# Performance work log

Hardware: AMD Instinct MI355X
Metric: run time of the kernel (lower is better)

## Reference

```python
import jax, jax.numpy as jnp
import numpy as np

EPS = 1e-5


def conv1d(x, w, b):
    # x: (B, C_in, S), w: (C_out, C_in, K), 'same' padding = K//2
    pad = w.shape[-1] // 2
    y = jax.lax.conv_general_dilated(
        x, w, window_strides=(1,), padding=[(pad, pad)],
        dimension_numbers=("NCH", "OIH", "NCH"))
    return y + b[None, :, None]


def layer_norm(x, g, b):
    m = jnp.mean(x, axis=-1, keepdims=True)
    v = jnp.var(x, axis=-1, keepdims=True)
    return (x - m) * jax.lax.rsqrt(v + EPS) * g + b


def duration_predict(x, conv1_w, conv1_b, conv2_w, conv2_b,
                     ln1_g, ln1_b, ln2_g, ln2_b, lin_w, lin_b):
    # x: (B, S, C)
    out = conv1d(jnp.swapaxes(x, -2, -1), conv1_w, conv1_b)          # (B, F, S)
    out = jax.nn.relu(layer_norm(jnp.swapaxes(out, -2, -1), ln1_g, ln1_b))  # (B, S, F)
    out = conv1d(jnp.swapaxes(out, -2, -1), conv2_w, conv2_b)        # (B, F, S)
    out = jax.nn.relu(layer_norm(jnp.swapaxes(out, -2, -1), ln2_g, ln2_b))  # (B, S, F)
    out = jax.nn.relu(out @ lin_w.T + lin_b)                          # (B, S, 1)
    return jnp.squeeze(out, -1)                                       # (B, S)


def setup_inputs() -> dict:
    key = jax.random.key(0)
    ks = jax.random.split(key, 6)
    B, S, C = 16, 1024, 256
    F_, K = 256, 3
    inp = {
        "x": jax.random.normal(ks[0], (B, S, C), dtype=jnp.float32),
        "target": jax.random.uniform(ks[1], (B, S), dtype=jnp.float32),
        "conv1_w": jax.random.normal(ks[2], (F_, C, K), dtype=jnp.float32) * 0.02,
        "conv1_b": jnp.zeros((F_,), dtype=jnp.float32),
        "conv2_w": jax.random.normal(ks[3], (F_, F_, K), dtype=jnp.float32) * 0.02,
        "conv2_b": jnp.zeros((F_,), dtype=jnp.float32),
        "ln1_g": jnp.ones((F_,), dtype=jnp.float32),
        "ln1_b": jnp.zeros((F_,), dtype=jnp.float32),
        "ln2_g": jnp.ones((F_,), dtype=jnp.float32),
        "ln2_b": jnp.zeros((F_,), dtype=jnp.float32),
        "lin_w": jax.random.normal(ks[4], (1, F_), dtype=jnp.float32) * 0.02,
        "lin_b": jnp.zeros((1,), dtype=jnp.float32),
    }
    return inp


def reference(x, target, conv1_w, conv1_b, conv2_w, conv2_b,
              ln1_g, ln1_b, ln2_g, ln2_b, lin_w, lin_b):
    reg_len = duration_predict(x, conv1_w, conv1_b, conv2_w, conv2_b,
                               ln1_g, ln1_b, ln2_g, ln2_b, lin_w, lin_b)
    # Faithful to the original: max_len uses exp(target), the mask uses round(target).
    # max_len is data-dependent -> computed from concrete target (host-side, like the original).
    max_len = int(np.round(float(jnp.max(jnp.sum(jnp.exp(target), axis=-1)))))
    d = jnp.round(target)                 # (B, S) integer-valued durations (banker's rounding, like Python round)
    fin = jnp.cumsum(d, axis=-1)          # (B, S) end offsets
    start = fin - d                       # (B, S) start offsets
    t = jnp.arange(max_len, dtype=target.dtype)  # (T,)
    mask = ((t[None, None, :] >= start[..., None]) &
            (t[None, None, :] < fin[..., None])).astype(x.dtype)  # (B, S, T)
    # x.transpose @ mask -> (B, C, T) -> transpose -> (B, T, C)
    expanded = jnp.einsum("bsc,bst->btc", x, mask)
    return expanded, reg_len
```

## Files before the change

### kernel.cpp

```cpp
#include <hip/hip_runtime.h>
#include <hip/hip_bf16.h>

using frag_ab = __attribute__((ext_vector_type(8))) short;
using frag_cd = __attribute__((ext_vector_type(4))) float;

#define SLEN 1024
#define CDIM 256
#define KTOT 768
#define PD 8

static __device__ __forceinline__ short f2bf(float f) {
    __hip_bfloat16 h = __float2bfloat16(f);
    return *reinterpret_cast<short*>(&h);
}

__global__ __launch_bounds__(1024) void scan_repack_kernel(
    const float* __restrict__ target, int* __restrict__ src, int T,
    const float* __restrict__ w1, __hip_bfloat16* __restrict__ bt1,
    const float* __restrict__ w2, __hip_bfloat16* __restrict__ bt2)
{
    __shared__ int waveSum[16];
    const int tid = threadIdx.x;

    if (blockIdx.x < 16) {
        const int b = blockIdx.x;
        for (int i = tid; i < T; i += 1024) src[b * T + i] = -1;

        const float tv = target[b * SLEN + tid];
        const int d = (int)rintf(tv);

        const int lane = tid & 63;
        const int wid = tid >> 6;
        int v = d;
#pragma unroll
        for (int off = 1; off < 64; off <<= 1) {
            int n = __shfl_up(v, off);
            if (lane >= off) v += n;
        }
        if (lane == 63) waveSum[wid] = v;
        __syncthreads();
        if (tid < 16) {
            int wv = waveSum[tid];
#pragma unroll
            for (int off = 1; off < 16; off <<= 1) {
                int n = __shfl_up(wv, off);
                if (tid >= off) wv += n;
            }
            waveSum[tid] = wv;
        }
        __syncthreads();
        const int fin = v + (wid > 0 ? waveSum[wid - 1] : 0);
        const int start = fin - d;
        for (int t = start; t < fin; ++t)
            if (t >= 0 && t < T) src[b * T + t] = tid;
    } else {
        const int id = (blockIdx.x - 16) * 1024 + tid;
        const int which = id >= 196608;
        const int e = which ? id - 196608 : id;
        const int f = e / KTOT;
        const int K = e - f * KTOT;
        const int k3 = K >> 8;
        const int c = K & 255;
        const float* w = which ? w2 : w1;
        __hip_bfloat16* bt = which ? bt2 : bt1;
        bt[f * KTOT + K] = __float2bfloat16(w[f * KTOT + c * 3 + k3]);
    }
}

__global__ __launch_bounds__(512, 2) void fused_conv_expand(
    const float* __restrict__ x,
    const __hip_bfloat16* __restrict__ bt1,
    const __hip_bfloat16* __restrict__ bt2,
    const float* __restrict__ cb1, const float* __restrict__ g1, const float* __restrict__ be1,
    const float* __restrict__ cb2, const float* __restrict__ g2, const float* __restrict__ be2,
    const float* __restrict__ lw, const float* __restrict__ lb,
    float* __restrict__ reg_len,
    const int* __restrict__ src, float* __restrict__ expanded, int T)
{
    __shared__ __align__(16) unsigned char xt[68 * 512];
    __shared__ __align__(16) unsigned char yt[66 * 512];
    __shared__ float red[66][17];
    __shared__ float stats[66][2];

    const int tid = threadIdx.x;
    const int lane = tid & 63;
    const int wid = tid >> 6;

    if (blockIdx.x >= 256) {
        const int row = (blockIdx.x - 256) * 8 + wid;
        const int nrows = 16 * T;
        if (row < nrows) {
            const int b = row / T;
            const int s = src[row];
            float4 val = make_float4(0.f, 0.f, 0.f, 0.f);
            if (s >= 0)
                val = *(const float4*)(x + ((size_t)(b * SLEN + s)) * CDIM + lane * 4);
            *(float4*)(expanded + (size_t)row * CDIM + lane * 4) = val;
        }
        return;
    }

    const int b = blockIdx.x >> 4;
    const int sx = blockIdx.x & 15;
    const int s0 = sx * 64;

    const int l15 = lane & 15;
    const int lk = lane >> 4;
    const int fbase = wid * 32;

    const __hip_bfloat16* p10 = bt1 + (size_t)(fbase + l15) * KTOT + lk * 8;
    const __hip_bfloat16* p11 = p10 + 16 * KTOT;
    frag_ab pb0[PD], pb1[PD];
#pragma unroll
    for (int i = 0; i < PD; ++i) {
        pb0[i] = *(const frag_ab*)(p10 + i * 32);
        pb1[i] = *(const frag_ab*)(p11 + i * 32);
    }

    const float* xin = x + (size_t)b * SLEN * CDIM;
    for (int ii = tid; ii < 68 * 32; ii += 512) {
        const int r = ii >> 5, cc = ii & 31;
        const int s = s0 - 2 + r;
        frag_ab v = {0, 0, 0, 0, 0, 0, 0, 0};
        if (s >= 0 && s < SLEN) {
            const float4* p = (const float4*)(xin + (size_t)s * CDIM + cc * 8);
            const float4 q0 = p[0], q1 = p[1];
            v[0] = f2bf(q0.x); v[1] = f2bf(q0.y); v[2] = f2bf(q0.z); v[3] = f2bf(q0.w);
            v[4] = f2bf(q1.x); v[5] = f2bf(q1.y); v[6] = f2bf(q1.z); v[7] = f2bf(q1.w);
        }
        *(frag_ab*)(xt + r * 512 + ((cc * 16) ^ ((r & 7) << 4))) = v;
    }
    __syncthreads();

    frag_cd acc1[5][2];
#pragma unroll
    for (int mf = 0; mf < 5; ++mf) {
        acc1[mf][0] = {0.f, 0.f, 0.f, 0.f};
        acc1[mf][1] = {0.f, 0.f, 0.f, 0.f};
    }
#pragma unroll
    for (int kk = 0; kk < 24; ++kk) {
        const frag_ab bb0 = pb0[kk % PD];
        const frag_ab bb1 = pb1[kk % PD];
        if (kk + PD < 24) {
            pb0[kk % PD] = *(const frag_ab*)(p10 + (kk + PD) * 32);
            pb1[kk % PD] = *(const frag_ab*)(p11 + (kk + PD) * 32);
        }
        const int k3 = kk >> 3;
        const int colbyte = (kk & 7) * 64 + lk * 16;
        frag_ab a[5];
#pragma unroll
        for (int mf = 0; mf < 5; ++mf) {
            int r = mf * 16 + l15 + k3;
            if (mf == 4) r = (r > 67) ? 67 : r;
            a[mf] = *(const frag_ab*)(xt + r * 512 + (colbyte ^ ((r & 7) << 4)));
        }
#pragma unroll
        for (int mf = 0; mf < 5; ++mf) {
            acc1[mf][0] = __builtin_amdgcn_mfma_f32_16x16x32_bf16(a[mf], bb0, acc1[mf][0], 0, 0, 0);
            acc1[mf][1] = __builtin_amdgcn_mfma_f32_16x16x32_bf16(a[mf], bb1, acc1[mf][1], 0, 0, 0);
        }
    }

    const __hip_bfloat16* p20 = bt2 + (size_t)(fbase + l15) * KTOT + lk * 8;
    const __hip_bfloat16* p21 = p20 + 16 * KTOT;
    frag_ab qb0[PD], qb1[PD];
#pragma unroll
    for (int i = 0; i < PD; ++i) {
        qb0[i] = *(const frag_ab*)(p20 + i * 32);
        qb1[i] = *(const frag_ab*)(p21 + i * 32);
    }

    {
        const float bias0 = cb1[fbase + l15];
        const float bias1 = cb1[fbase + 16 + l15];
#pragma unroll
        for (int mf = 0; mf < 5; ++mf) {
#pragma unroll
            for (int j = 0; j < 4; ++j) {
                acc1[mf][0][j] += bias0;
                acc1[mf][1][j] += bias1;
                float p = acc1[mf][0][j] + acc1[mf][1][j];
                float q = acc1[mf][0][j] * acc1[mf][0][j] + acc1[mf][1][j] * acc1[mf][1][j];
#pragma unroll
                for (int m = 1; m < 16; m <<= 1) {
                    p += __shfl_xor(p, m);
                    q += __shfl_xor(q, m);
                }
                const bool valid = (mf < 4) || (lk == 0 && j < 2);
                if (l15 == 0 && valid) {
                    const int yr = mf * 16 + lk * 4 + j;
                    red[yr][wid * 2] = p;
                    red[yr][wid * 2 + 1] = q;
                }
            }
        }
    }
    __syncthreads();
    if (tid < 66) {
        float s = 0.f, q = 0.f;
#pragma unroll
        for (int wv = 0; wv < 8; ++wv) { s += red[tid][wv * 2]; q += red[tid][wv * 2 + 1]; }
        const float mean = s * (1.f / 256.f);
        const float var = q * (1.f / 256.f) - mean * mean;
        stats[tid][0] = mean;
        stats[tid][1] = rsqrtf(var + 1e-5f);
    }
    __syncthreads();

    {
        const float ga0 = g1[fbase + l15], ga1 = g1[fbase + 16 + l15];
        const float bb0 = be1[fbase + l15], bb1 = be1[fbase + 16 + l15];
        const int c0b = (fbase + l15) * 2;
        const int c1b = (fbase + 16 + l15) * 2;
#pragma unroll
        for (int mf = 0; mf < 5; ++mf) {
#pragma unroll
            for (int j = 0; j < 4; ++j) {
                const bool valid = (mf < 4) || (lk == 0 && j < 2);
                if (valid) {
                    const int yr = mf * 16 + lk * 4 + j;
                    const float mean = stats[yr][0], rs = stats[yr][1];
                    float v0 = fmaxf((acc1[mf][0][j] - mean) * rs * ga0 + bb0, 0.f);
                    float v1 = fmaxf((acc1[mf][1][j] - mean) * rs * ga1 + bb1, 0.f);
                    const bool zrow = (sx == 0 && yr == 0) || (sx == 15 && yr == 65);
                    if (zrow) { v0 = 0.f; v1 = 0.f; }
                    const int sw = (yr & 7) << 4;
                    *(short*)(yt + yr * 512 + (c0b ^ sw)) = f2bf(v0);
                    *(short*)(yt + yr * 512 + (c1b ^ sw)) = f2bf(v1);
                }
            }
        }
    }
    __syncthreads();

    frag_cd acc2[4][2];
#pragma unroll
    for (int mf = 0; mf < 4; ++mf) {
        acc2[mf][0] = {0.f, 0.f, 0.f, 0.f};
        acc2[mf][1] = {0.f, 0.f, 0.f, 0.f};
    }
#pragma unroll
    for (int kk = 0; kk < 24; ++kk) {
        const frag_ab bb0 = qb0[kk % PD];
        const frag_ab bb1 = qb1[kk % PD];
        if (kk + PD < 24) {
            qb0[kk % PD] = *(const frag_ab*)(p20 + (kk + PD) * 32);
            qb1[kk % PD] = *(const frag_ab*)(p21 + (kk + PD) * 32);
        }
        const int k3 = kk >> 3;
        const int colbyte = (kk & 7) * 64 + lk * 16;
        frag_ab a[4];
#pragma unroll
        for (int mf = 0; mf < 4; ++mf) {
            const int r = mf * 16 + l15 + k3;
            a[mf] = *(const frag_ab*)(yt + r * 512 + (colbyte ^ ((r & 7) << 4)));
        }
#pragma unroll
        for (int mf = 0; mf < 4; ++mf) {
            acc2[mf][0] = __builtin_amdgcn_mfma_f32_16x16x32_bf16(a[mf], bb0, acc2[mf][0], 0, 0, 0);
            acc2[mf][1] = __builtin_amdgcn_mfma_f32_16x16x32_bf16(a[mf], bb1, acc2[mf][1], 0, 0, 0);
        }
    }

    {
        const float bias0 = cb2[fbase + l15];
        const float bias1 = cb2[fbase + 16 + l15];
#pragma unroll
        for (int mf = 0; mf < 4; ++mf) {
#pragma unroll
            for (int j = 0; j < 4; ++j) {
                acc2[mf][0][j] += bias0;
                acc2[mf][1][j] += bias1;
                float p = acc2[mf][0][j] + acc2[mf][1][j];
                float q = acc2[mf][0][j] * acc2[mf][0][j] + acc2[mf][1][j] * acc2[mf][1][j];
#pragma unroll
                for (int m = 1; m < 16; m <<= 1) {
                    p += __shfl_xor(p, m);
                    q += __shfl_xor(q, m);
                }
                if (l15 == 0) {
                    const int row = mf * 16 + lk * 4 + j;
                    red[row][wid * 2] = p;
                    red[row][wid * 2 + 1] = q;
                }
            }
        }
    }
    __syncthreads();
    if (tid < 64) {
        float s = 0.f, q = 0.f;
#pragma unroll
        for (int wv = 0; wv < 8; ++wv) { s += red[tid][wv * 2]; q += red[tid][wv * 2 + 1]; }
        const float mean = s * (1.f / 256.f);
        const float var = q * (1.f / 256.f) - mean * mean;
        stats[tid][0] = mean;
        stats[tid][1] = rsqrtf(var + 1e-5f);
    }
    __syncthreads();

    {
        const float ga0 = g2[fbase + l15], ga1 = g2[fbase + 16 + l15];
        const float bb0 = be2[fbase + l15], bb1 = be2[fbase + 16 + l15];
        const float lw0 = lw[fbase + l15], lw1 = lw[fbase + 16 + l15];
#pragma unroll
        for (int mf = 0; mf < 4; ++mf) {
#pragma unroll
            for (int j = 0; j < 4; ++j) {
                const int row = mf * 16 + lk * 4 + j;
                const float mean = stats[row][0], rs = stats[row][1];
                const float v0 = fmaxf((acc2[mf][0][j] - mean) * rs * ga0 + bb0, 0.f);
                const float v1 = fmaxf((acc2[mf][1][j] - mean) * rs * ga1 + bb1, 0.f);
                float p = v0 * lw0 + v1 * lw1;
#pragma unroll
                for (int m = 1; m < 16; m <<= 1) p += __shfl_xor(p, m);
                if (l15 == 0) red[row][wid * 2] = p;
            }
        }
    }
    __syncthreads();
    if (tid < 64) {
        float s = 0.f;
#pragma unroll
        for (int wv = 0; wv < 8; ++wv) s += red[tid][wv * 2];
        reg_len[b * SLEN + s0 + tid] = fmaxf(s + lb[0], 0.f);
    }
}

extern "C" void kernel_launch(void* const* d_in, const int* in_sizes, int n_in,
                              void* d_out, int out_size, void* d_ws, size_t ws_size,
                              hipStream_t stream)
{
    const float* x       = (const float*)d_in[0];
    const float* target  = (const float*)d_in[1];
    const float* conv1_w = (const float*)d_in[2];
    const float* conv1_b = (const float*)d_in[3];
    const float* conv2_w = (const float*)d_in[4];
    const float* conv2_b = (const float*)d_in[5];
    const float* ln1_g   = (const float*)d_in[6];
    const float* ln1_b   = (const float*)d_in[7];
    const float* ln2_g   = (const float*)d_in[8];
    const float* ln2_b   = (const float*)d_in[9];
    const float* lin_w   = (const float*)d_in[10];
    const float* lin_b   = (const float*)d_in[11];

    const int B = 16, S = 1024, C = 256;
    const int T = (out_size - B * S) / (B * C);

    float* expanded = (float*)d_out;
    float* reg_len  = (float*)d_out + (size_t)B * T * C;

    unsigned char* ws = (unsigned char*)d_ws;
    __hip_bfloat16* bt1 = (__hip_bfloat16*)ws;
    __hip_bfloat16* bt2 = (__hip_bfloat16*)(ws + 393216);
    int* src = (int*)(ws + 2 * 393216);

    scan_repack_kernel<<<400, 1024, 0, stream>>>(
        target, src, T, conv1_w, bt1, conv2_w, bt2);

    const int nExpBlocks = (B * T + 7) / 8;
    fused_conv_expand<<<256 + nExpBlocks, 512, 0, stream>>>(
        x, bt1, bt2, conv1_b, ln1_g, ln1_b, conv2_b, ln2_g, ln2_b,
        lin_w, lin_b, reg_len, src, expanded, T);
}
```

Before: 58.75 us.

## Overlap expand gather with conv compute via extra warp-specialized waves per block

Instead of launching separate expand blocks after the 256 conv blocks, each conv block gets 4 extra waves (768 threads) that perform the expand gather/copy in chunks interleaved between the conv phases' barriers. The aim is to hide the memory-bound expand traffic behind MFMA compute and drop the tail of extra blocks. In exchange, only 256 blocks now carry all of the expand work, the larger block size may lower occupancy, and every barrier waits for the slower expand chunks.

```diff
diff --git a/kernel.cpp b/kernel.cpp
--- a/kernel.cpp
+++ b/kernel.cpp
@@ -67,7 +67,7 @@
     }
 }
 
-__global__ __launch_bounds__(512, 2) void fused_conv_expand(
+__global__ __launch_bounds__(768, 3) void fused_conv_x(
     const float* __restrict__ x,
     const __hip_bfloat16* __restrict__ bt1,
     const __hip_bfloat16* __restrict__ bt2,
@@ -83,42 +83,53 @@
     __shared__ float stats[66][2];
 
     const int tid = threadIdx.x;
+    const int b = blockIdx.y;
+    const int s0 = blockIdx.x * 64;
+
     const int lane = tid & 63;
     const int wid = tid >> 6;
-
-    if (blockIdx.x >= 256) {
-        const int row = (blockIdx.x - 256) * 8 + wid;
-        const int nrows = 16 * T;
-        if (row < nrows) {
-            const int b = row / T;
-            const int s = src[row];
-            float4 val = make_float4(0.f, 0.f, 0.f, 0.f);
-            if (s >= 0)
-                val = *(const float4*)(x + ((size_t)(b * SLEN + s)) * CDIM + lane * 4);
-            *(float4*)(expanded + (size_t)row * CDIM + lane * 4) = val;
-        }
-        return;
-    }
-
-    const int b = blockIdx.x >> 4;
-    const int sx = blockIdx.x & 15;
-    const int s0 = sx * 64;
-
     const int l15 = lane & 15;
     const int lk = lane >> 4;
-    const int fbase = wid * 32;
+    const int fbase = (wid & 7) * 32;
+
+    const int nrows = 16 * T;
+    const int rpb = (nrows + 255) >> 8;
+    const int rpw = (rpb + 3) >> 2;
+    const int csz = (rpw + 3) >> 2;
+    const int erow0 = (b * 16 + blockIdx.x) * rpb + (wid - 8) * rpw;
+
+    auto expand_chunk = [&](int c) {
+        const int i0 = c * csz;
+        const int i1 = (i0 + csz < rpw) ? i0 + csz : rpw;
+        for (int i = i0; i < i1; ++i) {
+            const int row = erow0 + i;
+            if (row < nrows) {
+                const int bb = row / T;
+                const int s = src[row];
+                float4 val = make_float4(0.f, 0.f, 0.f, 0.f);
+                if (s >= 0)
+                    val = *(const float4*)(x + ((size_t)(bb * SLEN + s)) * CDIM + lane * 4);
+                *(float4*)(expanded + (size_t)row * CDIM + lane * 4) = val;
+            }
+        }
+    };
 
     const __hip_bfloat16* p10 = bt1 + (size_t)(fbase + l15) * KTOT + lk * 8;
     const __hip_bfloat16* p11 = p10 + 16 * KTOT;
+    const __hip_bfloat16* p20 = bt2 + (size_t)(fbase + l15) * KTOT + lk * 8;
+    const __hip_bfloat16* p21 = p20 + 16 * KTOT;
+
     frag_ab pb0[PD], pb1[PD];
-#pragma unroll
-    for (int i = 0; i < PD; ++i) {
-        pb0[i] = *(const frag_ab*)(p10 + i * 32);
-        pb1[i] = *(const frag_ab*)(p11 + i * 32);
+    if (wid < 8) {
+#pragma unroll
+        for (int i = 0; i < PD; ++i) {
+            pb0[i] = *(const frag_ab*)(p10 + i * 32);
+            pb1[i] = *(const frag_ab*)(p11 + i * 32);
+        }
     }
 
     const float* xin = x + (size_t)b * SLEN * CDIM;
-    for (int ii = tid; ii < 68 * 32; ii += 512) {
+    for (int ii = tid; ii < 68 * 32; ii += 768) {
         const int r = ii >> 5, cc = ii & 31;
         const int s = s0 - 2 + r;
         frag_ab v = {0, 0, 0, 0, 0, 0, 0, 0};
@@ -133,45 +144,44 @@
     __syncthreads();
 
     frag_cd acc1[5][2];
-#pragma unroll
-    for (int mf = 0; mf < 5; ++mf) {
-        acc1[mf][0] = {0.f, 0.f, 0.f, 0.f};
-        acc1[mf][1] = {0.f, 0.f, 0.f, 0.f};
-    }
-#pragma unroll
-    for (int kk = 0; kk < 24; ++kk) {
-        const frag_ab bb0 = pb0[kk % PD];
-        const frag_ab bb1 = pb1[kk % PD];
-        if (kk + PD < 24) {
-            pb0[kk % PD] = *(const frag_ab*)(p10 + (kk + PD) * 32);
-            pb1[kk % PD] = *(const frag_ab*)(p11 + (kk + PD) * 32);
-        }
-        const int k3 = kk >> 3;
-        const int colbyte = (kk & 7) * 64 + lk * 16;
-        frag_ab a[5];
+    frag_cd acc2[4][2];
+    frag_ab qb0[PD], qb1[PD];
+    if (wid < 8) {
 #pragma unroll
         for (int mf = 0; mf < 5; ++mf) {
-            int r = mf * 16 + l15 + k3;
-            if (mf == 4) r = (r > 67) ? 67 : r;
-            a[mf] = *(const frag_ab*)(xt + r * 512 + (colbyte ^ ((r & 7) << 4)));
-        }
-#pragma unroll
-        for (int mf = 0; mf < 5; ++mf) {
-            acc1[mf][0] = __builtin_amdgcn_mfma_f32_16x16x32_bf16(a[mf], bb0, acc1[mf][0], 0, 0, 0);
-            acc1[mf][1] = __builtin_amdgcn_mfma_f32_16x16x32_bf16(a[mf], bb1, acc1[mf][1], 0, 0, 0);
-        }
-    }
-
-    const __hip_bfloat16* p20 = bt2 + (size_t)(fbase + l15) * KTOT + lk * 8;
-    const __hip_bfloat16* p21 = p20 + 16 * KTOT;
-    frag_ab qb0[PD], qb1[PD];
-#pragma unroll
-    for (int i = 0; i < PD; ++i) {
-        qb0[i] = *(const frag_ab*)(p20 + i * 32);
-        qb1[i] = *(const frag_ab*)(p21 + i * 32);
-    }
-
-    {
+            acc1[mf][0] = {0.f, 0.f, 0.f, 0.f};
+            acc1[mf][1] = {0.f, 0.f, 0.f, 0.f};
+        }
+#pragma unroll
+        for (int kk = 0; kk < 24; ++kk) {
+            const frag_ab bb0 = pb0[kk % PD];
+            const frag_ab bb1 = pb1[kk % PD];
+            if (kk + PD < 24) {
+                pb0[kk % PD] = *(const frag_ab*)(p10 + (kk + PD) * 32);
+                pb1[kk % PD] = *(const frag_ab*)(p11 + (kk + PD) * 32);
+            }
+            const int k3 = kk >> 3;
+            const int colbyte = (kk & 7) * 64 + lk * 16;
+            frag_ab a[5];
+#pragma unroll
+            for (int mf = 0; mf < 5; ++mf) {
+                int r = mf * 16 + l15 + k3;
+                if (mf == 4) r = (r > 67) ? 67 : r;
+                a[mf] = *(const frag_ab*)(xt + r * 512 + (colbyte ^ ((r & 7) << 4)));
+            }
+#pragma unroll
+            for (int mf = 0; mf < 5; ++mf) {
+                acc1[mf][0] = __builtin_amdgcn_mfma_f32_16x16x32_bf16(a[mf], bb0, acc1[mf][0], 0, 0, 0);
+                acc1[mf][1] = __builtin_amdgcn_mfma_f32_16x16x32_bf16(a[mf], bb1, acc1[mf][1], 0, 0, 0);
+            }
+        }
+
+#pragma unroll
+        for (int i = 0; i < PD; ++i) {
+            qb0[i] = *(const frag_ab*)(p20 + i * 32);
+            qb1[i] = *(const frag_ab*)(p21 + i * 32);
+        }
+
         const float bias0 = cb1[fbase + l15];
         const float bias1 = cb1[fbase + 16 + l15];
 #pragma unroll
@@ -195,6 +205,8 @@
                 }
             }
         }
+    } else {
+        expand_chunk(0);
     }
     __syncthreads();
     if (tid < 66) {
@@ -208,7 +220,7 @@
     }
     __syncthreads();
 
-    {
+    if (wid < 8) {
         const float ga0 = g1[fbase + l15], ga1 = g1[fbase + 16 + l15];
         const float bb0 = be1[fbase + l15], bb1 = be1[fbase + 16 + l15];
         const int c0b = (fbase + l15) * 2;
@@ -223,7 +235,8 @@
                     const float mean = stats[yr][0], rs = stats[yr][1];
                     float v0 = fmaxf((acc1[mf][0][j] - mean) * rs * ga0 + bb0, 0.f);
                     float v1 = fmaxf((acc1[mf][1][j] - mean) * rs * ga1 + bb1, 0.f);
-                    const bool zrow = (sx == 0 && yr == 0) || (sx == 15 && yr == 65);
+                    const bool zrow = (blockIdx.x == 0 && yr == 0) ||
+                                      (blockIdx.x == 15 && yr == 65);
                     if (zrow) { v0 = 0.f; v1 = 0.f; }
                     const int sw = (yr & 7) << 4;
                     *(short*)(yt + yr * 512 + (c0b ^ sw)) = f2bf(v0);
@@ -231,39 +244,40 @@
                 }
             }
         }
-    }
-    __syncthreads();
-
-    frag_cd acc2[4][2];
-#pragma unroll
-    for (int mf = 0; mf < 4; ++mf) {
-        acc2[mf][0] = {0.f, 0.f, 0.f, 0.f};
-        acc2[mf][1] = {0.f, 0.f, 0.f, 0.f};
-    }
-#pragma unroll
-    for (int kk = 0; kk < 24; ++kk) {
-        const frag_ab bb0 = qb0[kk % PD];
-        const frag_ab bb1 = qb1[kk % PD];
-        if (kk + PD < 24) {
-            qb0[kk % PD] = *(const frag_ab*)(p20 + (kk + PD) * 32);
-            qb1[kk % PD] = *(const frag_ab*)(p21 + (kk + PD) * 32);
-        }
-        const int k3 = kk >> 3;
-        const int colbyte = (kk & 7) * 64 + lk * 16;
-        frag_ab a[4];
+    } else {
+        expand_chunk(1);
+    }
+    __syncthreads();
+
+    if (wid < 8) {
 #pragma unroll
         for (int mf = 0; mf < 4; ++mf) {
-            const int r = mf * 16 + l15 + k3;
-            a[mf] = *(const frag_ab*)(yt + r * 512 + (colbyte ^ ((r & 7) << 4)));
-        }
-#pragma unroll
-        for (int mf = 0; mf < 4; ++mf) {
-            acc2[mf][0] = __builtin_amdgcn_mfma_f32_16x16x32_bf16(a[mf], bb0, acc2[mf][0], 0, 0, 0);
-            acc2[mf][1] = __builtin_amdgcn_mfma_f32_16x16x32_bf16(a[mf], bb1, acc2[mf][1], 0, 0, 0);
-        }
-    }
-
-    {
+            acc2[mf][0] = {0.f, 0.f, 0.f, 0.f};
+            acc2[mf][1] = {0.f, 0.f, 0.f, 0.f};
+        }
+#pragma unroll
+        for (int kk = 0; kk < 24; ++kk) {
+            const frag_ab bb0 = qb0[kk % PD];
+            const frag_ab bb1 = qb1[kk % PD];
+            if (kk + PD < 24) {
+                qb0[kk % PD] = *(const frag_ab*)(p20 + (kk + PD) * 32);
+                qb1[kk % PD] = *(const frag_ab*)(p21 + (kk + PD) * 32);
+            }
+            const int k3 = kk >> 3;
+            const int colbyte = (kk & 7) * 64 + lk * 16;
+            frag_ab a[4];
+#pragma unroll
+            for (int mf = 0; mf < 4; ++mf) {
+                const int r = mf * 16 + l15 + k3;
+                a[mf] = *(const frag_ab*)(yt + r * 512 + (colbyte ^ ((r & 7) << 4)));
+            }
+#pragma unroll
+            for (int mf = 0; mf < 4; ++mf) {
+                acc2[mf][0] = __builtin_amdgcn_mfma_f32_16x16x32_bf16(a[mf], bb0, acc2[mf][0], 0, 0, 0);
+                acc2[mf][1] = __builtin_amdgcn_mfma_f32_16x16x32_bf16(a[mf], bb1, acc2[mf][1], 0, 0, 0);
+            }
+        }
+
         const float bias0 = cb2[fbase + l15];
         const float bias1 = cb2[fbase + 16 + l15];
 #pragma unroll
@@ -286,6 +300,8 @@
                 }
             }
         }
+    } else {
+        expand_chunk(2);
     }
     __syncthreads();
     if (tid < 64) {
@@ -299,7 +315,7 @@
     }
     __syncthreads();
 
-    {
+    if (wid < 8) {
         const float ga0 = g2[fbase + l15], ga1 = g2[fbase + 16 + l15];
         const float bb0 = be2[fbase + l15], bb1 = be2[fbase + 16 + l15];
         const float lw0 = lw[fbase + l15], lw1 = lw[fbase + 16 + l15];
@@ -317,6 +333,8 @@
                 if (l15 == 0) red[row][wid * 2] = p;
             }
         }
+    } else {
+        expand_chunk(3);
     }
     __syncthreads();
     if (tid < 64) {
@@ -358,8 +376,7 @@
     scan_repack_kernel<<<400, 1024, 0, stream>>>(
         target, src, T, conv1_w, bt1, conv2_w, bt2);
 
-    const int nExpBlocks = (B * T + 7) / 8;
-    fused_conv_expand<<<256 + nExpBlocks, 512, 0, stream>>>(
+    fused_conv_x<<<dim3(16, 16), 768, 0, stream>>>(
         x, bt1, bt2, conv1_b, ln1_g, ln1_b, conv2_b, ln2_g, ln2_b,
         lin_w, lin_b, reg_len, src, expanded, T);
 }
```

Measured after the change: 65.21 us. 1.11x slower.
